# Kernel tuning notes

Measured on AMD Instinct MI355X. Metric: run time of the kernel, lower is better.

## Reference

```python
import jax, jax.numpy as jnp
import numpy as np


def setup_inputs() -> dict:
    T, B, D = 2048, 8, 1024
    key = jax.random.key(0)
    k1, k2, k3 = jax.random.split(key, 3)
    # xavier-uniform-ish scale for [D, D] weights
    lim = float(np.sqrt(6.0 / (D + D)))
    return {
        "x": jax.random.normal(k1, (T, B, D), dtype=jnp.float32),
        "h0": jnp.zeros((B, D), dtype=jnp.float32),
        "W_alpha": jax.random.uniform(k2, (D, D), dtype=jnp.float32, minval=-lim, maxval=lim),
        "b_alpha": jnp.full((D,), 2.0, dtype=jnp.float32),  # init_alpha_bias
        "W_x": jax.random.uniform(k3, (D, D), dtype=jnp.float32, minval=-lim, maxval=lim),
        "b": jnp.zeros((D,), dtype=jnp.float32),
    }


def reference(x, h0, W_alpha, b_alpha, W_x, b):
    # Precompute input projections for all timesteps (one big GEMM each).
    # alpha_t = sigmoid(W_alpha @ x_t + b_alpha); v_t = tanh(h_{t-1} + W_x @ x_t + b)
    alpha_all = jax.nn.sigmoid(jnp.einsum('tbd,ed->tbe', x, W_alpha) + b_alpha)  # [T,B,D]
    wx_all = jnp.einsum('tbd,ed->tbe', x, W_x) + b                                # [T,B,D]

    def step(h_prev, inp):
        alpha, wx = inp
        v = jnp.tanh(h_prev + wx)
        h_new = alpha * h_prev + (1.0 - alpha) * v
        out = h_new * jax.nn.silu(h_new)
        return h_new, (out, h_new)

    _, (output, hs) = jax.lax.scan(step, h0, (alpha_all, wx_all))
    h = jnp.concatenate([h0[None], hs], axis=0)  # [T+1, B, D]
    return output, h
```

## Files before the change

kernel.cpp:

```cpp
#include <hip/hip_runtime.h>
#include <hip/hip_bf16.h>
#include <cstdint>
#include <cstddef>

#define T_STEPS 2048
#define BATCH   8
#define D_DIM   1024
#define M_ROWS  (T_STEPS * BATCH)
#define N_COLS  (2 * D_DIM)
#define K_DIM   D_DIM
#define NCH     (BATCH * D_DIM)

#define BM 128
#define BN 128
#define BK 32

typedef __bf16 bf16x8 __attribute__((ext_vector_type(8)));
typedef float  f32x4  __attribute__((ext_vector_type(4)));

__device__ __forceinline__ unsigned short f2bf_rne(float f) {
    union { float f; unsigned u; } c; c.f = f;
    unsigned u = c.u;
    u += 0x7fffu + ((u >> 16) & 1u);
    return (unsigned short)(u >> 16);
}

__device__ __forceinline__ float sigmoid_f(float z) {
    return 1.0f / (1.0f + __expf(-z));
}

__device__ __forceinline__ void glds16(const void* gptr, void* lptr) {
    __builtin_amdgcn_global_load_lds(
        (const __attribute__((address_space(1))) unsigned int*)gptr,
        (__attribute__((address_space(3))) unsigned int*)lptr,
        16, 0, 0);
}

__global__ void cvt_bf16_kernel(const float* __restrict__ src,
                                unsigned short* __restrict__ dst, int n4) {
    int i = blockIdx.x * blockDim.x + threadIdx.x;
    if (i >= n4) return;
    float4 v = reinterpret_cast<const float4*>(src)[i];
    ushort4 o;
    o.x = f2bf_rne(v.x); o.y = f2bf_rne(v.y);
    o.z = f2bf_rne(v.z); o.w = f2bf_rne(v.w);
    reinterpret_cast<ushort4*>(dst)[i] = o;
}

__global__ __launch_bounds__(256, 2)
void gemm_kernel(const unsigned short* __restrict__ A,
                 const unsigned short* __restrict__ Bm,
                 const float* __restrict__ b_alpha,
                 const float* __restrict__ b_x,
                 float* __restrict__ alpha_out,
                 float* __restrict__ wx_out)
{
    __shared__ unsigned short sA[BM * BK];
    __shared__ unsigned short sB[BN * BK];

    const int tid  = threadIdx.x;
    const int wave = tid >> 6;
    const int lane = tid & 63;
    const int rowBase = blockIdx.y * BM;
    const int colBase = blockIdx.x * BN;
    const int wr = (wave >> 1) * 64;
    const int wc = (wave & 1) * 64;

    const int laneHi = lane >> 4;
    const int laneLo = lane & 15;

    const int dRow = lane >> 2;
    const int dCol = (lane & 3) * 8;

    f32x4 acc[4][4];
#pragma unroll
    for (int i = 0; i < 4; i++)
#pragma unroll
        for (int j = 0; j < 4; j++)
            acc[i][j] = (f32x4)(0.0f);

    for (int k0 = 0; k0 < K_DIM; k0 += BK) {
#pragma unroll
        for (int p = 0; p < 2; ++p) {
            const int seg = wave * 2 + p;
            glds16(A + (size_t)(rowBase + seg * 16 + dRow) * K_DIM + k0 + dCol,
                   &sA[seg * 512]);
            glds16(Bm + (size_t)(colBase + seg * 16 + dRow) * K_DIM + k0 + dCol,
                   &sB[seg * 512]);
        }
        __syncthreads();

        bf16x8 af[4], bfr[4];
#pragma unroll
        for (int i = 0; i < 4; i++)
            af[i] = *reinterpret_cast<const bf16x8*>(
                &sA[(wr + i * 16 + laneLo) * BK + laneHi * 8]);
#pragma unroll
        for (int j = 0; j < 4; j++)
            bfr[j] = *reinterpret_cast<const bf16x8*>(
                &sB[(wc + j * 16 + laneLo) * BK + laneHi * 8]);
        __syncthreads();

#pragma unroll
        for (int i = 0; i < 4; i++)
#pragma unroll
            for (int j = 0; j < 4; j++)
                acc[i][j] = __builtin_amdgcn_mfma_f32_16x16x32_bf16(
                    af[i], bfr[j], acc[i][j], 0, 0, 0);
    }

#pragma unroll
    for (int i = 0; i < 4; i++) {
        int row = rowBase + wr + i * 16 + laneHi * 4;
#pragma unroll
        for (int j = 0; j < 4; j++) {
            int col = colBase + wc + j * 16 + laneLo;
            if (col < D_DIM) {
                float bias = b_alpha[col];
#pragma unroll
                for (int r = 0; r < 4; r++) {
                    float z = acc[i][j][r] + bias;
                    alpha_out[(size_t)(row + r) * D_DIM + col] = sigmoid_f(z);
                }
            } else {
                int c2 = col - D_DIM;
                float bias = b_x[c2];
#pragma unroll
                for (int r = 0; r < 4; r++)
                    wx_out[(size_t)(row + r) * D_DIM + c2] = acc[i][j][r] + bias;
            }
        }
    }
}

#define TT 32
#define NT (T_STEPS / TT)
#define CPB 128

__global__ __launch_bounds__(128)
void scan_kernel(const float* __restrict__ alpha,
                 const float* __restrict__ wx,
                 const float* __restrict__ h0,
                 float* __restrict__ hout)
{
    __shared__ float sAl[2][TT * CPB];
    __shared__ float sWx[2][TT * CPB];

    const int lane = threadIdx.x & 63;
    const int wave = threadIdx.x >> 6;
    const int ch0  = blockIdx.x * CPB;

    const int q  = lane >> 5;
    const int c4 = (lane & 31) * 4;

    const float C2L = 2.88539008177792681472f;

    float hA = 0.0f, hB = 0.0f;

    if (wave == 1) {
#pragma unroll
        for (int p = 0; p < TT / 2; ++p) {
            const size_t g = (size_t)(p * 2 + q) * NCH + ch0 + c4;
            glds16(alpha + g, &sAl[0][p * 256]);
            glds16(wx    + g, &sWx[0][p * 256]);
        }
    } else {
        const float2 h2 = *reinterpret_cast<const float2*>(&h0[ch0 + 2 * lane]);
        hA = h2.x; hB = h2.y;
        *reinterpret_cast<float2*>(&hout[ch0 + 2 * lane]) = h2;
    }
    __syncthreads();

    for (int tile = 0; tile < NT; ++tile) {
        const int cur = tile & 1;
        if (wave == 1) {
            if (tile + 1 < NT) {
                const int t0 = (tile + 1) * TT;
#pragma unroll
                for (int p = 0; p < TT / 2; ++p) {
                    const size_t g = (size_t)(t0 + p * 2 + q) * NCH + ch0 + c4;
                    glds16(alpha + g, &sAl[cur ^ 1][p * 256]);
                    glds16(wx    + g, &sWx[cur ^ 1][p * 256]);
                }
            }
        } else {
            const int tbase = tile * TT;
#pragma unroll 16
            for (int ts = 0; ts < TT; ++ts) {
                const float2 a2 = *reinterpret_cast<const float2*>(
                    &sAl[cur][ts * CPB + 2 * lane]);
                const float2 w2 = *reinterpret_cast<const float2*>(
                    &sWx[cur][ts * CPB + 2 * lane]);
                const float uA = 1.0f - a2.x;
                const float pA = fmaf(hA, C2L, w2.x * C2L);
                const float eA = __builtin_amdgcn_exp2f(pA);
                const float rA = __builtin_amdgcn_rcpf(eA + 1.0f);
                const float mA = fmaf(a2.x, hA, uA);
                hA = fmaf(-(uA + uA), rA, mA);
                const float uB = 1.0f - a2.y;
                const float pB = fmaf(hB, C2L, w2.y * C2L);
                const float eB = __builtin_amdgcn_exp2f(pB);
                const float rB = __builtin_amdgcn_rcpf(eB + 1.0f);
                const float mB = fmaf(a2.y, hB, uB);
                hB = fmaf(-(uB + uB), rB, mB);

                const int t = tbase + ts;
                *reinterpret_cast<float2*>(
                    &hout[(size_t)(t + 1) * NCH + ch0 + 2 * lane]) =
                    make_float2(hA, hB);
            }
        }
        __syncthreads();
    }
}

__global__ __launch_bounds__(256)
void out_kernel(const float* __restrict__ hnext,
                float* __restrict__ out, int n4) {
    const float L2E = 1.44269504088896340736f;
    int stride = gridDim.x * blockDim.x;
    for (int i = blockIdx.x * blockDim.x + threadIdx.x; i < n4; i += stride) {
        float4 h = reinterpret_cast<const float4*>(hnext)[i];
        float4 o;
        o.x = h.x * h.x * __builtin_amdgcn_rcpf(1.0f + __builtin_amdgcn_exp2f(-L2E * h.x));
        o.y = h.y * h.y * __builtin_amdgcn_rcpf(1.0f + __builtin_amdgcn_exp2f(-L2E * h.y));
        o.z = h.z * h.z * __builtin_amdgcn_rcpf(1.0f + __builtin_amdgcn_exp2f(-L2E * h.z));
        o.w = h.w * h.w * __builtin_amdgcn_rcpf(1.0f + __builtin_amdgcn_exp2f(-L2E * h.w));
        reinterpret_cast<float4*>(out)[i] = o;
    }
}

extern "C" void kernel_launch(void* const* d_in, const int* in_sizes, int n_in,
                              void* d_out, int out_size, void* d_ws, size_t ws_size,
                              hipStream_t stream) {
    const float* x       = (const float*)d_in[0];
    const float* h0      = (const float*)d_in[1];
    const float* W_alpha = (const float*)d_in[2];
    const float* b_alpha = (const float*)d_in[3];
    const float* W_x     = (const float*)d_in[4];
    const float* b       = (const float*)d_in[5];

    float* out  = (float*)d_out;
    float* hout = out + (size_t)T_STEPS * BATCH * D_DIM;

    float* ws_alpha = (float*)d_ws;
    float* ws_wx    = ws_alpha + (size_t)M_ROWS * D_DIM;
    unsigned short* ws_x = (unsigned short*)(ws_wx + (size_t)M_ROWS * D_DIM);
    unsigned short* ws_W = ws_x + (size_t)M_ROWS * K_DIM;

    {
        int n4 = M_ROWS * K_DIM / 4;
        cvt_bf16_kernel<<<(n4 + 255) / 256, 256, 0, stream>>>(x, ws_x, n4);
    }
    {
        int n4 = D_DIM * K_DIM / 4;
        cvt_bf16_kernel<<<(n4 + 255) / 256, 256, 0, stream>>>(W_alpha, ws_W, n4);
        cvt_bf16_kernel<<<(n4 + 255) / 256, 256, 0, stream>>>(
            W_x, ws_W + (size_t)D_DIM * K_DIM, n4);
    }

    {
        dim3 grid(N_COLS / BN, M_ROWS / BM);
        gemm_kernel<<<grid, 256, 0, stream>>>(ws_x, ws_W, b_alpha, b,
                                              ws_alpha, ws_wx);
    }

    scan_kernel<<<NCH / CPB, 128, 0, stream>>>(ws_alpha, ws_wx, h0, hout);

    {
        int n4 = (int)((size_t)T_STEPS * NCH / 4);
        out_kernel<<<2048, 256, 0, stream>>>(hout + NCH, out, n4);
    }
}
```

Measured before the change: 405.7 us.

## Replace LDS double-buffered scan with per-lane register prefetch pipeline

New measurement: 425.1 us. +4.8%, slower.

```diff
diff --git a/kernel.cpp b/kernel.cpp
--- a/kernel.cpp
+++ b/kernel.cpp
@@ -133,84 +133,49 @@
     }
 }
 
-#define TT 32
-#define NT (T_STEPS / TT)
-#define CPB 128
-
-__global__ __launch_bounds__(128)
+#define DEPTH 16
+
+__global__ __launch_bounds__(64)
 void scan_kernel(const float* __restrict__ alpha,
                  const float* __restrict__ wx,
                  const float* __restrict__ h0,
                  float* __restrict__ hout)
 {
-    __shared__ float sAl[2][TT * CPB];
-    __shared__ float sWx[2][TT * CPB];
-
-    const int lane = threadIdx.x & 63;
-    const int wave = threadIdx.x >> 6;
-    const int ch0  = blockIdx.x * CPB;
-
-    const int q  = lane >> 5;
-    const int c4 = (lane & 31) * 4;
+    const int lane = threadIdx.x;
+    const int ch   = blockIdx.x * 64 + lane;
 
     const float C2L = 2.88539008177792681472f;
 
-    float hA = 0.0f, hB = 0.0f;
-
-    if (wave == 1) {
-#pragma unroll
-        for (int p = 0; p < TT / 2; ++p) {
-            const size_t g = (size_t)(p * 2 + q) * NCH + ch0 + c4;
-            glds16(alpha + g, &sAl[0][p * 256]);
-            glds16(wx    + g, &sWx[0][p * 256]);
+    const float* ap = alpha + ch;
+    const float* wp = wx + ch;
+    float* hp = hout + NCH + ch;
+
+    float aP[DEPTH], wP[DEPTH];
+#pragma unroll
+    for (int d = 0; d < DEPTH; ++d) {
+        aP[d] = ap[(size_t)d * NCH];
+        wP[d] = wp[(size_t)d * NCH];
+    }
+
+    float h = h0[ch];
+    hout[ch] = h;
+
+    for (int t0 = 0; t0 < T_STEPS; t0 += DEPTH) {
+#pragma unroll
+        for (int d = 0; d < DEPTH; ++d) {
+            const float a = aP[d];
+            const float w = wP[d];
+            const size_t tn = (size_t)(t0 + DEPTH + d);
+            aP[d] = ap[tn * NCH];
+            wP[d] = wp[tn * NCH];
+            const float u = 1.0f - a;
+            const float p = fmaf(h, C2L, w * C2L);
+            const float e = __builtin_amdgcn_exp2f(p);
+            const float r = __builtin_amdgcn_rcpf(e + 1.0f);
+            const float m = fmaf(a, h, u);
+            h = fmaf(-(u + u), r, m);
+            hp[(size_t)(t0 + d) * NCH] = h;
         }
-    } else {
-        const float2 h2 = *reinterpret_cast<const float2*>(&h0[ch0 + 2 * lane]);
-        hA = h2.x; hB = h2.y;
-        *reinterpret_cast<float2*>(&hout[ch0 + 2 * lane]) = h2;
-    }
-    __syncthreads();
-
-    for (int tile = 0; tile < NT; ++tile) {
-        const int cur = tile & 1;
-        if (wave == 1) {
-            if (tile + 1 < NT) {
-                const int t0 = (tile + 1) * TT;
-#pragma unroll
-                for (int p = 0; p < TT / 2; ++p) {
-                    const size_t g = (size_t)(t0 + p * 2 + q) * NCH + ch0 + c4;
-                    glds16(alpha + g, &sAl[cur ^ 1][p * 256]);
-                    glds16(wx    + g, &sWx[cur ^ 1][p * 256]);
-                }
-            }
-        } else {
-            const int tbase = tile * TT;
-#pragma unroll 16
-            for (int ts = 0; ts < TT; ++ts) {
-                const float2 a2 = *reinterpret_cast<const float2*>(
-                    &sAl[cur][ts * CPB + 2 * lane]);
-                const float2 w2 = *reinterpret_cast<const float2*>(
-                    &sWx[cur][ts * CPB + 2 * lane]);
-                const float uA = 1.0f - a2.x;
-                const float pA = fmaf(hA, C2L, w2.x * C2L);
-                const float eA = __builtin_amdgcn_exp2f(pA);
-                const float rA = __builtin_amdgcn_rcpf(eA + 1.0f);
-                const float mA = fmaf(a2.x, hA, uA);
-                hA = fmaf(-(uA + uA), rA, mA);
-                const float uB = 1.0f - a2.y;
-                const float pB = fmaf(hB, C2L, w2.y * C2L);
-                const float eB = __builtin_amdgcn_exp2f(pB);
-                const float rB = __builtin_amdgcn_rcpf(eB + 1.0f);
-                const float mB = fmaf(a2.y, hB, uB);
-                hB = fmaf(-(uB + uB), rB, mB);
-
-                const int t = tbase + ts;
-                *reinterpret_cast<float2*>(
-                    &hout[(size_t)(t + 1) * NCH + ch0 + 2 * lane]) =
-                    make_float2(hA, hB);
-            }
-        }
-        __syncthreads();
     }
 }
 
@@ -265,7 +230,7 @@
                                               ws_alpha, ws_wx);
     }
 
-    scan_kernel<<<NCH / CPB, 128, 0, stream>>>(ws_alpha, ws_wx, h0, hout);
+    scan_kernel<<<NCH / 64, 64, 0, stream>>>(ws_alpha, ws_wx, h0, hout);
 
     {
         int n4 = (int)((size_t)T_STEPS * NCH / 4);
```
